# Performance work log

Hardware: AMD Instinct MI355X
Metric: run time of the kernel (lower is better)

Reference implementation:

```python
import jax, jax.numpy as jnp
import numpy as np

# DenseCRF hyperparameters (match init_kwargs)
NUM_CLASS = 21
H, W = 96, 96
APP_W, SMO_W = 10.0, 3.0          # appearance_weight, smoothness_weight
PROX_STD, COLOR_STD, SMOOTH_STD = 30.0, 0.1, 3.0
ITERS = 5


def setup_inputs() -> dict:
    key = jax.random.key(0)
    k1, k2 = jax.random.split(key)
    x = jax.random.uniform(k1, (3, H, W), dtype=jnp.float32)        # RGB image in [0,1]
    yhat = jax.random.normal(k2, (NUM_CLASS, H, W), dtype=jnp.float32)  # logits
    # Potts-model incompatibility matrix: ones - eye
    mu = jnp.ones((NUM_CLASS, NUM_CLASS), jnp.float32) - jnp.eye(NUM_CLASS, dtype=jnp.float32)
    return {"x": x, "yhat": yhat, "mu": mu}


def _gauss_kernel(feats):
    """Exact Gaussian kernel K_ij = exp(-||f_i - f_j||^2 / 2), feats: (N, D).
    This is the math the permutohedral lattice splat/blur/slice approximates."""
    sq = jnp.sum(feats * feats, axis=1)                 # (N,)
    d2 = sq[:, None] + sq[None, :] - 2.0 * feats @ feats.T  # (N, N)
    return jnp.exp(-0.5 * jnp.maximum(d2, 0.0))


def reference(x, yhat, mu):
    C, Hh, Ww = yhat.shape
    # pixel coordinate grid, (2, H, W)
    yy, xx = jnp.mgrid[0:Hh, 0:Ww]
    pos = jnp.stack([yy, xx]).astype(jnp.float32)
    # bilateral features: (y, x, r, g, b) scaled by per-dim sigmas -> (N, 5)
    sig_bi = jnp.array([PROX_STD, PROX_STD, COLOR_STD, COLOR_STD, COLOR_STD], jnp.float32)
    f_bi = jnp.concatenate([pos, x], axis=0).reshape(5, -1).T / sig_bi
    # smoothness features: (y, x) / smoothness_std -> (N, 2)
    f_sm = pos.reshape(2, -1).T / SMOOTH_STD
    # "fit": build the filtering kernels once
    K_bi = _gauss_kernel(f_bi)   # (N, N)
    K_sm = _gauss_kernel(f_sm)   # (N, N)

    unary = yhat.reshape(C, -1)                 # (C, N)
    out = jax.nn.softmax(unary, axis=0)
    for _ in range(ITERS):
        app = K_bi @ out.T                      # (N, C) bilateral message passing
        smo = K_sm @ out.T                      # (N, C) spatial message passing
        pw = APP_W * app + SMO_W * smo          # (N, C)
        # einsum('ij,bi->bj', mu, pw).T  ==  (pw @ mu).T
        pw = (pw @ mu).T                        # (C, N) compatibility transform
        unary = unary + pw
        out = jax.nn.softmax(unary, axis=0)
    return out.reshape(C, Hh, Ww)
```

## Files before the change

kernel.cpp:

```cpp
#include <hip/hip_runtime.h>
#include <math.h>


#define NN 9216
#define CC 21
#define HH 96
#define WW 96
#define CP 24
#define JS2 12
#define NJ2 (NN / JS2)
#define TJ2 128
#define OST2 136

typedef _Float16 half8 __attribute__((ext_vector_type(8)));
typedef __fp16 fp16x2 __attribute__((ext_vector_type(2)));
typedef float f32x4 __attribute__((ext_vector_type(4)));

union HU { int i[4]; half8 h; };

__global__ __launch_bounds__(256) void featinit_kernel(const float* __restrict__ x,
                                                       const float* __restrict__ yhat,
                                                       float* __restrict__ feat,
                                                       float* __restrict__ unary,
                                                       _Float16* __restrict__ out_hi,
                                                       _Float16* __restrict__ out_lo,
                                                       float* __restrict__ out_cn) {
    int n = blockIdx.x * 256 + threadIdx.x;
    {
        int y = n / WW, xx = n - y * WW;
        const float inv_sqrt_ln2 = 1.2011224087864498f;
        float sp = inv_sqrt_ln2 / 30.0f;
        float sc = inv_sqrt_ln2 * 10.0f;
        float fy = (float)y * sp;
        float fx = (float)xx * sp;
        float fr = x[0 * NN + n] * sc;
        float fg = x[1 * NN + n] * sc;
        float fb = x[2 * NN + n] * sc;
        float S = fy * fy + fx * fx + fr * fr + fg * fg + fb * fb;
        float4* f4 = (float4*)(feat + (size_t)n * 8);
        f4[0] = make_float4(fy, fx, fr, fg);
        f4[1] = make_float4(fb, -0.5f * S, 0.0f, 0.0f);
    }
    float u[CC], p[CC];
    float m = -1e30f;
#pragma unroll
    for (int c = 0; c < CC; c++) { u[c] = yhat[c * NN + n]; m = fmaxf(m, u[c]); }
    float s = 0.0f;
#pragma unroll
    for (int c = 0; c < CC; c++) { p[c] = __expf(u[c] - m); s += p[c]; }
    float inv = 1.0f / s;
#pragma unroll
    for (int c = 0; c < CC; c++) p[c] *= inv;
#pragma unroll
    for (int c = 0; c < CC; c++) {
        unary[n * CP + c] = u[c];
        _Float16 ph = (_Float16)p[c];
        out_hi[(size_t)c * NN + n] = ph;
        out_lo[(size_t)c * NN + n] = (_Float16)(p[c] - (float)ph);
        out_cn[c * NN + n] = p[c];
    }
#pragma unroll
    for (int c = CC; c < CP; c++) {
        unary[n * CP + c] = 0.0f;
        out_hi[(size_t)c * NN + n] = (_Float16)0.0f;
        out_lo[(size_t)c * NN + n] = (_Float16)0.0f;
    }
}

__global__ __launch_bounds__(256, 4) void bilateral_mfma(const float* __restrict__ feat,
                                                         const _Float16* __restrict__ out_hi,
                                                         const _Float16* __restrict__ out_lo,
                                                         float* __restrict__ part) {
    __shared__ float smemf[4288];
    float* sfeat = smemf;
    _Float16* sh_ = (_Float16*)(smemf + 1024);
    _Float16* sl_ = (_Float16*)(smemf + 2656);

    const int tid = threadIdx.x;
    const int lane = tid & 63;
    const int w = tid >> 6;
    const int r = lane & 15;
    const int g = lane >> 4;
    const int i0 = blockIdx.x * 64;
    const int jslice = blockIdx.y * NJ2;

    float fi0[4], fi1[4], fi2[4], fi3[4], fi4[4], hsi[4];
#pragma unroll
    for (int m = 0; m < 4; ++m) {
        const float* fp = feat + (size_t)(i0 + m * 16 + r) * 8;
        float4 A = *(const float4*)fp;
        float2 B = *(const float2*)(fp + 4);
        fi0[m] = A.x; fi1[m] = A.y; fi2[m] = A.z; fi3[m] = A.w;
        fi4[m] = B.x; hsi[m] = B.y;
    }

    f32x4 acc[4][2];
#pragma unroll
    for (int m = 0; m < 4; ++m) { acc[m][0] = (f32x4)0.0f; acc[m][1] = (f32x4)0.0f; }

    const int jb = w * 32 + g * 8;
    const int r2 = (r < 8) ? (16 + r) : 23;

#pragma unroll 1
    for (int rd = 0; rd < NJ2 / TJ2; ++rd) {
        __syncthreads();
        {
            int j = tid >> 1, h = tid & 1;
            int jp = j ^ ((j >> 3) & 3);
            ((float4*)sfeat)[jp * 2 + h] =
                *(const float4*)(feat + (size_t)(jslice + rd * TJ2 + j) * 8 + h * 4);
        }
        for (int v = tid; v < 768; v += 256) {
            int vv = v;
            _Float16* dstbase;
            const _Float16* srcbase;
            if (vv < 384) { dstbase = sh_; srcbase = out_hi; }
            else { dstbase = sl_; srcbase = out_lo; vv -= 384; }
            int c = vv >> 4, j8 = vv & 15;
            *(float4*)(dstbase + c * OST2 + j8 * 8) =
                *(const float4*)(srcbase + (size_t)c * NN + jslice + rd * TJ2 + j8 * 8);
        }
        __syncthreads();

        int wh[4][4], wl[4][4];
#pragma unroll
        for (int tp = 0; tp < 4; ++tp) {
            const float* jp0 = sfeat + (size_t)(w * 32 + g * 8 + ((2 * tp) ^ g)) * 8;
            const float* jp1 = sfeat + (size_t)(w * 32 + g * 8 + ((2 * tp + 1) ^ g)) * 8;
            float4 A0 = *(const float4*)jp0;
            float2 B0 = *(const float2*)(jp0 + 4);
            float4 A1 = *(const float4*)jp1;
            float2 B1 = *(const float2*)(jp1 + 4);
#pragma unroll
            for (int m = 0; m < 4; ++m) {
                float d0 = hsi[m] + B0.y;
                d0 = fmaf(fi0[m], A0.x, d0);
                d0 = fmaf(fi1[m], A0.y, d0);
                d0 = fmaf(fi2[m], A0.z, d0);
                d0 = fmaf(fi3[m], A0.w, d0);
                d0 = fmaf(fi4[m], B0.x, d0);
                float d1 = hsi[m] + B1.y;
                d1 = fmaf(fi0[m], A1.x, d1);
                d1 = fmaf(fi1[m], A1.y, d1);
                d1 = fmaf(fi2[m], A1.z, d1);
                d1 = fmaf(fi3[m], A1.w, d1);
                d1 = fmaf(fi4[m], B1.x, d1);
                float k0 = __builtin_amdgcn_exp2f(d0);
                float k1 = __builtin_amdgcn_exp2f(d1);
                fp16x2 kh = __builtin_amdgcn_cvt_pkrtz(k0, k1);
                fp16x2 kl = __builtin_amdgcn_cvt_pkrtz(k0 - (float)kh.x,
                                                       k1 - (float)kh.y);
                __builtin_memcpy(&wh[m][tp], &kh, 4);
                __builtin_memcpy(&wl[m][tp], &kl, 4);
            }
        }
        half8 b0h = *(const half8*)(sh_ + r * OST2 + jb);
        half8 b0l = *(const half8*)(sl_ + r * OST2 + jb);
        half8 b1h = *(const half8*)(sh_ + r2 * OST2 + jb);
        half8 b1l = *(const half8*)(sl_ + r2 * OST2 + jb);
#pragma unroll
        for (int m = 0; m < 4; ++m) {
            HU uh, ul;
            uh.i[0] = wh[m][0]; uh.i[1] = wh[m][1];
            uh.i[2] = wh[m][2]; uh.i[3] = wh[m][3];
            ul.i[0] = wl[m][0]; ul.i[1] = wl[m][1];
            ul.i[2] = wl[m][2]; ul.i[3] = wl[m][3];
            acc[m][0] = __builtin_amdgcn_mfma_f32_16x16x32_f16(uh.h, b0h, acc[m][0], 0, 0, 0);
            acc[m][0] = __builtin_amdgcn_mfma_f32_16x16x32_f16(ul.h, b0h, acc[m][0], 0, 0, 0);
            acc[m][0] = __builtin_amdgcn_mfma_f32_16x16x32_f16(uh.h, b0l, acc[m][0], 0, 0, 0);
            acc[m][1] = __builtin_amdgcn_mfma_f32_16x16x32_f16(uh.h, b1h, acc[m][1], 0, 0, 0);
            acc[m][1] = __builtin_amdgcn_mfma_f32_16x16x32_f16(ul.h, b1h, acc[m][1], 0, 0, 0);
            acc[m][1] = __builtin_amdgcn_mfma_f32_16x16x32_f16(uh.h, b1l, acc[m][1], 0, 0, 0);
        }
    }

#pragma unroll
    for (int m = 0; m < 4; ++m) {
        __syncthreads();
        if (w != m) {
            float* dst = smemf + (size_t)(w * 64 + lane) * 12;
            *(f32x4*)(dst + 0) = acc[m][0];
            *(f32x4*)(dst + 4) = acc[m][1];
        }
        __syncthreads();
        if (w == m) {
            f32x4 s0 = acc[m][0], s1 = acc[m][1];
#pragma unroll
            for (int k = 0; k < 4; ++k) {
                if (k == m) continue;
                const float* src = smemf + (size_t)(k * 64 + lane) * 12;
                s0 += *(const f32x4*)(src + 0);
                s1 += *(const f32x4*)(src + 4);
            }
            float* pb = part + ((size_t)blockIdx.y * NN + i0 + m * 16 + g * 4) * 32 + r;
#pragma unroll
            for (int q = 0; q < 4; ++q) {
                pb[q * 32] = s0[q];
                pb[q * 32 + 16] = s1[q];
            }
        }
    }
}

__global__ __launch_bounds__(256) void smo_y_kernel(const float* __restrict__ src,
                                                    float* __restrict__ dst) {
    __shared__ float wt[2 * HH - 1];
    int tid = threadIdx.x;
    if (tid < 2 * HH - 1) {
        float d = (float)(tid - (HH - 1));
        wt[tid] = __expf(d * d * (-1.0f / 18.0f));
    }
    __syncthreads();
    int id = blockIdx.x * 256 + tid;
    int c = id / NN;
    int rem = id - c * NN;
    int y = rem / WW;
    int x = rem - y * WW;
    const float* s = src + (size_t)c * NN + x;
    float a = 0.0f;
    for (int yp = 0; yp < HH; yp++) a = fmaf(wt[yp - y + (HH - 1)], s[yp * WW], a);
    dst[id] = a;
}

__global__ __launch_bounds__(256) void smo_x_kernel(const float* __restrict__ src,
                                                    float* __restrict__ dst) {
    __shared__ float wt[2 * HH - 1];
    int tid = threadIdx.x;
    if (tid < 2 * HH - 1) {
        float d = (float)(tid - (HH - 1));
        wt[tid] = __expf(d * d * (-1.0f / 18.0f));
    }
    __syncthreads();
    int id = blockIdx.x * 256 + tid;
    int c = id / NN;
    int rem = id - c * NN;
    int y = rem / WW;
    int x = rem - y * WW;
    const float* s = src + (size_t)c * NN + y * WW;
    float a = 0.0f;
    for (int xp = 0; xp < WW; xp++) a = fmaf(wt[xp - x + (HH - 1)], s[xp], a);
    dst[id] = a;
}

__global__ __launch_bounds__(256) void combine_kernel(const float* __restrict__ part,
                                                      const float* __restrict__ smo,
                                                      const float* __restrict__ mu,
                                                      float* __restrict__ unary,
                                                      _Float16* __restrict__ out_hi,
                                                      _Float16* __restrict__ out_lo,
                                                      float* __restrict__ out_cn) {
    __shared__ float muL[CC * CC];
    int tid = threadIdx.x;
    for (int u = tid; u < CC * CC; u += 256) muL[u] = mu[u];
    __syncthreads();
    int n = blockIdx.x * 256 + tid;
    float app[32];
#pragma unroll
    for (int c = 0; c < 32; c++) app[c] = 0.0f;
    for (int k = 0; k < JS2; k++) {
        const float4* p4 = (const float4*)(part + ((size_t)k * NN + n) * 32);
#pragma unroll
        for (int q = 0; q < 8; q++) {
            float4 v = p4[q];
            app[q * 4 + 0] += v.x;
            app[q * 4 + 1] += v.y;
            app[q * 4 + 2] += v.z;
            app[q * 4 + 3] += v.w;
        }
    }
    float pin[CC];
#pragma unroll
    for (int c = 0; c < CC; c++) pin[c] = 10.0f * app[c] + 3.0f * smo[c * NN + n];
    float pout[CC];
#pragma unroll
    for (int j = 0; j < CC; j++) pout[j] = 0.0f;
#pragma unroll
    for (int i2 = 0; i2 < CC; i2++) {
        float v = pin[i2];
#pragma unroll
        for (int j = 0; j < CC; j++) pout[j] = fmaf(v, muL[i2 * CC + j], pout[j]);
    }
    float u[CC], p[CC];
    float m = -1e30f;
#pragma unroll
    for (int c = 0; c < CC; c++) {
        u[c] = unary[n * CP + c] + pout[c];
        m = fmaxf(m, u[c]);
    }
    float s = 0.0f;
#pragma unroll
    for (int c = 0; c < CC; c++) { p[c] = __expf(u[c] - m); s += p[c]; }
    float inv = 1.0f / s;
#pragma unroll
    for (int c = 0; c < CC; c++) p[c] *= inv;
#pragma unroll
    for (int c = 0; c < CC; c++) {
        unary[n * CP + c] = u[c];
        _Float16 ph = (_Float16)p[c];
        out_hi[(size_t)c * NN + n] = ph;
        out_lo[(size_t)c * NN + n] = (_Float16)(p[c] - (float)ph);
        out_cn[c * NN + n] = p[c];
    }
}

extern "C" void kernel_launch(void* const* d_in, const int* in_sizes, int n_in,
                              void* d_out, int out_size, void* d_ws, size_t ws_size,
                              hipStream_t stream) {
    const float* x = (const float*)d_in[0];
    const float* yhat = (const float*)d_in[1];
    const float* mu = (const float*)d_in[2];
    float* out = (float*)d_out;
    float* ws = (float*)d_ws;

    float*     feat   = ws;
    _Float16*  out_hi = (_Float16*)(ws + 73728);
    _Float16*  out_lo = (_Float16*)(ws + 184320);
    float*     unary  = ws + 294912;
    float*     smo    = ws + 516096;
    float*     tmp    = ws + 709632;
    float*     part   = ws + 903168;

    featinit_kernel<<<NN / 256, 256, 0, stream>>>(x, yhat, feat, unary, out_hi, out_lo, out);

    for (int it = 0; it < 5; it++) {
        bilateral_mfma<<<dim3(144, JS2), 256, 0, stream>>>(feat, out_hi, out_lo, part);
        smo_y_kernel<<<CC * NN / 256, 256, 0, stream>>>(out, tmp);
        smo_x_kernel<<<CC * NN / 256, 256, 0, stream>>>(tmp, smo);
        combine_kernel<<<NN / 256, 256, 0, stream>>>(part, smo, mu, unary, out_hi, out_lo, out);
    }
}
```

Baseline: 366.9 us.

## Fuse horizontal smoothing pass into combine and use channel-major partial layout

```diff
diff --git a/kernel.cpp b/kernel.cpp
--- a/kernel.cpp
+++ b/kernel.cpp
@@ -15,6 +15,7 @@
 typedef _Float16 half8 __attribute__((ext_vector_type(8)));
 typedef __fp16 fp16x2 __attribute__((ext_vector_type(2)));
 typedef float f32x4 __attribute__((ext_vector_type(4)));
+typedef float f32x2 __attribute__((ext_vector_type(2)));
 
 union HU { int i[4]; half8 h; };
 
@@ -131,22 +132,18 @@
             float2 B0 = *(const float2*)(jp0 + 4);
             float4 A1 = *(const float4*)jp1;
             float2 B1 = *(const float2*)(jp1 + 4);
+            f32x2 ax = {A0.x, A1.x}, ay = {A0.y, A1.y}, az = {A0.z, A1.z};
+            f32x2 aw = {A0.w, A1.w}, bx = {B0.x, B1.x}, hby = {B0.y, B1.y};
 #pragma unroll
             for (int m = 0; m < 4; ++m) {
-                float d0 = hsi[m] + B0.y;
-                d0 = fmaf(fi0[m], A0.x, d0);
-                d0 = fmaf(fi1[m], A0.y, d0);
-                d0 = fmaf(fi2[m], A0.z, d0);
-                d0 = fmaf(fi3[m], A0.w, d0);
-                d0 = fmaf(fi4[m], B0.x, d0);
-                float d1 = hsi[m] + B1.y;
-                d1 = fmaf(fi0[m], A1.x, d1);
-                d1 = fmaf(fi1[m], A1.y, d1);
-                d1 = fmaf(fi2[m], A1.z, d1);
-                d1 = fmaf(fi3[m], A1.w, d1);
-                d1 = fmaf(fi4[m], B1.x, d1);
-                float k0 = __builtin_amdgcn_exp2f(d0);
-                float k1 = __builtin_amdgcn_exp2f(d1);
+                f32x2 d = hby + hsi[m];
+                d = d + ax * fi0[m];
+                d = d + ay * fi1[m];
+                d = d + az * fi2[m];
+                d = d + aw * fi3[m];
+                d = d + bx * fi4[m];
+                float k0 = __builtin_amdgcn_exp2f(d[0]);
+                float k1 = __builtin_amdgcn_exp2f(d[1]);
                 fp16x2 kh = __builtin_amdgcn_cvt_pkrtz(k0, k1);
                 fp16x2 kl = __builtin_amdgcn_cvt_pkrtz(k0 - (float)kh.x,
                                                        k1 - (float)kh.y);
@@ -192,11 +189,13 @@
                 s0 += *(const f32x4*)(src + 0);
                 s1 += *(const f32x4*)(src + 4);
             }
-            float* pb = part + ((size_t)blockIdx.y * NN + i0 + m * 16 + g * 4) * 32 + r;
-#pragma unroll
-            for (int q = 0; q < 4; ++q) {
-                pb[q * 32] = s0[q];
-                pb[q * 32 + 16] = s1[q];
+            float* pb0 = part + ((size_t)blockIdx.y * CC + r) * NN + i0 + m * 16 + g * 4;
+#pragma unroll
+            for (int q = 0; q < 4; ++q) pb0[q] = s0[q];
+            if (r < 5) {
+                float* pb1 = part + ((size_t)blockIdx.y * CC + 16 + r) * NN + i0 + m * 16 + g * 4;
+#pragma unroll
+                for (int q = 0; q < 4; ++q) pb1[q] = s1[q];
             }
         }
     }
@@ -222,55 +221,37 @@
     dst[id] = a;
 }
 
-__global__ __launch_bounds__(256) void smo_x_kernel(const float* __restrict__ src,
-                                                    float* __restrict__ dst) {
-    __shared__ float wt[2 * HH - 1];
-    int tid = threadIdx.x;
-    if (tid < 2 * HH - 1) {
-        float d = (float)(tid - (HH - 1));
-        wt[tid] = __expf(d * d * (-1.0f / 18.0f));
-    }
-    __syncthreads();
-    int id = blockIdx.x * 256 + tid;
-    int c = id / NN;
-    int rem = id - c * NN;
-    int y = rem / WW;
-    int x = rem - y * WW;
-    const float* s = src + (size_t)c * NN + y * WW;
-    float a = 0.0f;
-    for (int xp = 0; xp < WW; xp++) a = fmaf(wt[xp - x + (HH - 1)], s[xp], a);
-    dst[id] = a;
-}
-
 __global__ __launch_bounds__(256) void combine_kernel(const float* __restrict__ part,
-                                                      const float* __restrict__ smo,
+                                                      const float* __restrict__ tmp,
                                                       const float* __restrict__ mu,
                                                       float* __restrict__ unary,
                                                       _Float16* __restrict__ out_hi,
                                                       _Float16* __restrict__ out_lo,
                                                       float* __restrict__ out_cn) {
     __shared__ float muL[CC * CC];
+    __shared__ float wt[2 * HH - 1];
     int tid = threadIdx.x;
     for (int u = tid; u < CC * CC; u += 256) muL[u] = mu[u];
+    if (tid < 2 * HH - 1) {
+        float d = (float)(tid - (HH - 1));
+        wt[tid] = __expf(d * d * (-1.0f / 18.0f));
+    }
     __syncthreads();
     int n = blockIdx.x * 256 + tid;
-    float app[32];
-#pragma unroll
-    for (int c = 0; c < 32; c++) app[c] = 0.0f;
-    for (int k = 0; k < JS2; k++) {
-        const float4* p4 = (const float4*)(part + ((size_t)k * NN + n) * 32);
-#pragma unroll
-        for (int q = 0; q < 8; q++) {
-            float4 v = p4[q];
-            app[q * 4 + 0] += v.x;
-            app[q * 4 + 1] += v.y;
-            app[q * 4 + 2] += v.z;
-            app[q * 4 + 3] += v.w;
-        }
-    }
+    int y = n / WW;
+    int x = n - y * WW;
+
     float pin[CC];
 #pragma unroll
-    for (int c = 0; c < CC; c++) pin[c] = 10.0f * app[c] + 3.0f * smo[c * NN + n];
+    for (int c = 0; c < CC; c++) {
+        float a = 0.0f;
+#pragma unroll
+        for (int k = 0; k < JS2; k++) a += part[((size_t)k * CC + c) * NN + n];
+        const float* s = tmp + (size_t)c * NN + y * WW;
+        float sm = 0.0f;
+        for (int xp = 0; xp < WW; xp++) sm = fmaf(wt[xp - x + (HH - 1)], s[xp], sm);
+        pin[c] = 10.0f * a + 3.0f * sm;
+    }
     float pout[CC];
 #pragma unroll
     for (int j = 0; j < CC; j++) pout[j] = 0.0f;
@@ -316,16 +297,14 @@
     _Float16*  out_hi = (_Float16*)(ws + 73728);
     _Float16*  out_lo = (_Float16*)(ws + 184320);
     float*     unary  = ws + 294912;
-    float*     smo    = ws + 516096;
-    float*     tmp    = ws + 709632;
-    float*     part   = ws + 903168;
+    float*     tmp    = ws + 516096;
+    float*     part   = ws + 709632;
 
     featinit_kernel<<<NN / 256, 256, 0, stream>>>(x, yhat, feat, unary, out_hi, out_lo, out);
 
     for (int it = 0; it < 5; it++) {
         bilateral_mfma<<<dim3(144, JS2), 256, 0, stream>>>(feat, out_hi, out_lo, part);
         smo_y_kernel<<<CC * NN / 256, 256, 0, stream>>>(out, tmp);
-        smo_x_kernel<<<CC * NN / 256, 256, 0, stream>>>(tmp, smo);
-        combine_kernel<<<NN / 256, 256, 0, stream>>>(part, smo, mu, unary, out_hi, out_lo, out);
-    }
-}
+        combine_kernel<<<NN / 256, 256, 0, stream>>>(part, tmp, mu, unary, out_hi, out_lo, out);
+    }
+}
```

Result: slower. 464.8 us (+26.7%).
